# Performance work log

Hardware: AMD Instinct MI355X
Metric: run time of the kernel (lower is better)

The kernel has to match this reference:

```python
import jax, jax.numpy as jnp
import numpy as np

T, D, F_, E, K = 8192, 1024, 4096, 8, 2


def setup_inputs() -> dict:
    key = jax.random.key(0)
    ks = jax.random.split(key, 5)
    s_d = 1.0 / np.sqrt(D)
    s_f = 1.0 / np.sqrt(F_)
    return {
        "x": jax.random.normal(ks[0], (T, D), dtype=jnp.float32),
        "gate_w": jax.random.normal(ks[1], (D, E), dtype=jnp.float32) * s_d,
        "w1": jax.random.normal(ks[2], (E, D, F_), dtype=jnp.float32) * s_d,  # up (gate proj)
        "w3": jax.random.normal(ks[3], (E, D, F_), dtype=jnp.float32) * s_d,  # up (value proj)
        "w2": jax.random.normal(ks[4], (E, F_, D), dtype=jnp.float32) * s_f,  # down proj
    }


def reference(x, gate_w, w1, w2, w3):
    # gate + top-k routing
    logits = x @ gate_w                                   # [T, E]
    top_w, top_idx = jax.lax.top_k(logits, K)             # [T, K]
    w = jax.nn.softmax(top_w.astype(jnp.float32), axis=-1).astype(x.dtype)
    # combine[t, e] = routing weight of token t for expert e (0 if unrouted)
    combine = jnp.sum(w[:, :, None] * jax.nn.one_hot(top_idx, E, dtype=x.dtype), axis=1)  # [T, E]
    # dense dispatch: each expert processes all tokens, masked by combine weight
    # (identical math to the torch gather/scatter loop: unrouted tokens get weight 0)
    out = jnp.zeros_like(x)
    for e in range(E):
        h = jax.nn.silu(x @ w1[e]) * (x @ w3[e])          # [T, F] SwiGLU
        out = out + combine[:, e:e + 1] * (h @ w2[e])     # [T, D]
    return out
```

## Files before the change

kernel.cpp:

```cpp
#include <hip/hip_runtime.h>
#include <stdint.h>

#define T_TOK 8192
#define D_DIM 1024
#define F_DIM 4096
#define E_NUM 8
#define RCAP  17408
#define MT    136

typedef __bf16 bf16;
typedef __bf16 bf16x8 __attribute__((ext_vector_type(8)));
typedef float  f32x4  __attribute__((ext_vector_type(4)));

typedef const __attribute__((address_space(1))) void* gptr1;
typedef __attribute__((address_space(3))) void* lptr3;

__device__ __forceinline__ void gload_lds16(const void* g, void* l) {
    __builtin_amdgcn_global_load_lds((gptr1)g, (lptr3)l, 16, 0, 0);
}

__device__ __forceinline__ unsigned short f2b(float f) {
    uint32_t u = __float_as_uint(f);
    u = (u + 0x7FFFu + ((u >> 16) & 1u)) >> 16;
    return (unsigned short)u;
}

__global__ __launch_bounds__(256) void trans_kernel(const float* __restrict__ src,
                                                    bf16* __restrict__ dst,
                                                    int R, int C, int mode) {
    __shared__ float lt[64 * 68];
    const int e  = blockIdx.z;
    const int c0 = blockIdx.x * 64;
    const int r0 = blockIdx.y * 64;
    const float* s = src + (size_t)e * R * C;
    unsigned short* dp = (unsigned short*)dst + (size_t)e * R * C * (mode ? 2 : 1);
    const int t  = threadIdx.x;
    const int tr = t >> 4;
    const int tc = (t & 15) * 4;
    #pragma unroll
    for (int rr = 0; rr < 4; ++rr) {
        const int r = tr + rr * 16;
        const float4 v = *(const float4*)(s + (size_t)(r0 + r) * C + c0 + tc);
        *(float4*)&lt[r * 68 + tc] = v;
    }
    __syncthreads();
    const int oc  = t >> 2;
    const int seg = (t & 3) * 16;
    __attribute__((aligned(16))) unsigned short ob[16];
    #pragma unroll
    for (int i = 0; i < 16; ++i) ob[i] = f2b(lt[(seg + i) * 68 + oc]);
    const int f  = c0 + oc;
    const int fr = mode ? ((f >> 5) * 64 + ((mode == 2) ? 32 : 0) + (f & 31)) : f;
    unsigned short* orow = dp + (size_t)fr * R + (r0 + seg);
    *(uint4*)(orow)     = *(const uint4*)&ob[0];
    *(uint4*)(orow + 8) = *(const uint4*)&ob[8];
}

__global__ __launch_bounds__(256) void gate_kernel(const float* __restrict__ x,
                                                   const float* __restrict__ gw,
                                                   int* __restrict__ tki,
                                                   float* __restrict__ tkw,
                                                   int* __restrict__ counts) {
    const int t    = blockIdx.x * 4 + (threadIdx.x >> 6);
    const int lane = threadIdx.x & 63;
    const float* xr = x + (size_t)t * D_DIM;
    float acc[E_NUM];
    #pragma unroll
    for (int e = 0; e < E_NUM; ++e) acc[e] = 0.f;
    for (int j = 0; j < 16; ++j) {
        const int d = lane + 64 * j;
        const float xv = xr[d];
        const float* g = gw + (size_t)d * E_NUM;
        #pragma unroll
        for (int e = 0; e < E_NUM; ++e) acc[e] += xv * g[e];
    }
    #pragma unroll
    for (int off = 32; off >= 1; off >>= 1) {
        #pragma unroll
        for (int e = 0; e < E_NUM; ++e) acc[e] += __shfl_xor(acc[e], off);
    }
    if (lane == 0) {
        int b0 = 0; float v0 = acc[0];
        #pragma unroll
        for (int e = 1; e < E_NUM; ++e) if (acc[e] > v0) { v0 = acc[e]; b0 = e; }
        int b1 = -1; float v1 = -1e30f;
        #pragma unroll
        for (int e = 0; e < E_NUM; ++e) if (e != b0 && acc[e] > v1) { v1 = acc[e]; b1 = e; }
        const float ex = expf(v1 - v0);
        const float w0 = 1.f / (1.f + ex);
        const float w1 = ex * w0;
        tki[t * 2]     = b0;  tkw[t * 2]     = w0;
        tki[t * 2 + 1] = b1;  tkw[t * 2 + 1] = w1;
        atomicAdd(&counts[b0], 1);
        atomicAdd(&counts[b1], 1);
    }
}

__global__ void scan_kernel(const int* __restrict__ counts, int* __restrict__ aoff,
                            int* __restrict__ cursor) {
    if (threadIdx.x == 0) {
        int off = 0;
        #pragma unroll
        for (int e = 0; e < E_NUM; ++e) {
            aoff[e]   = off;
            cursor[e] = off;
            off += (counts[e] + 127) & ~127;
        }
        aoff[E_NUM] = off;
    }
}

__global__ __launch_bounds__(256) void gather_kernel(const float* __restrict__ x,
                                                     const int* __restrict__ tki,
                                                     int* __restrict__ cursor,
                                                     int* __restrict__ s2r,
                                                     bf16* __restrict__ xp) {
    const int slot = blockIdx.x * 4 + (threadIdx.x >> 6);
    const int lane = threadIdx.x & 63;
    const int t = slot >> 1;
    int row = 0;
    if (lane == 0) {
        const int e = tki[slot];
        row = atomicAdd(&cursor[e], 1);
        s2r[slot] = row;
    }
    row = __shfl(row, 0);
    const float* xr = x + (size_t)t * D_DIM + lane * 16;
    unsigned short* dst = (unsigned short*)xp + (size_t)row * D_DIM + lane * 16;
    uint32_t u[8];
    #pragma unroll
    for (int q = 0; q < 4; ++q) {
        const float4 v = *(const float4*)(xr + q * 4);
        u[q * 2]     = (uint32_t)f2b(v.x) | ((uint32_t)f2b(v.y) << 16);
        u[q * 2 + 1] = (uint32_t)f2b(v.z) | ((uint32_t)f2b(v.w) << 16);
    }
    ((uint4*)dst)[0] = make_uint4(u[0], u[1], u[2], u[3]);
    ((uint4*)dst)[1] = make_uint4(u[4], u[5], u[6], u[7]);
}

__global__ __launch_bounds__(512, 2) void gemm1_kernel(const bf16* __restrict__ xp,
                                                       const bf16* __restrict__ wb13t,
                                                       bf16* __restrict__ hb,
                                                       const int* __restrict__ aoff,
                                                       const int* __restrict__ counts) {
    __shared__ __align__(16) char As[65536];
    __shared__ __align__(16) char Bs[65536];

    const int nt = blockIdx.x;
    int bm = blockIdx.y;
    int e  = 0;
    for (; e < E_NUM; ++e) {
        const int nbi = (counts[e] + 255) >> 8;
        if (bm < nbi) break;
        bm -= nbi;
    }
    if (e >= E_NUM) return;
    const int m_base = aoff[e] + bm * 256;
    const int row_hi = aoff[e + 1];

    const int tid  = threadIdx.x;
    const int w    = tid >> 6;
    const int lane = tid & 63;
    const int wm   = w >> 2;
    const int wn   = w & 3;

    const int    lsub = lane >> 3;
    const size_t swz  = (size_t)(((lane & 7) ^ lsub) << 3);
    const bf16* Ag = xp    + (size_t)m_base * D_DIM;
    const bf16* Bg = wb13t + ((size_t)e * (2 * F_DIM) + (size_t)nt * 256) * D_DIM;
    char* sAd = As + w * 2048 + lane * 16;
    char* sBd = Bs + w * 2048 + lane * 16;
    const int rst = w * 16 + lsub;

#define G1_STAGE_A(cc, kt, h)                                                         \
    do {                                                                              \
        const size_t kcol = (size_t)(kt) * 64 + swz;                                  \
        gload_lds16(Ag + (size_t)((h) * 128 + rst) * D_DIM + kcol,                    \
                    sAd + (cc) * 32768 + (h) * 16384);                                \
        gload_lds16(Ag + (size_t)((h) * 128 + rst + 8) * D_DIM + kcol,                \
                    sAd + (cc) * 32768 + (h) * 16384 + 1024);                         \
    } while (0)
#define G1_STAGE_B(cc, kt, h)                                                         \
    do {                                                                              \
        const size_t kcol = (size_t)(kt) * 64 + swz;                                  \
        gload_lds16(Bg + (size_t)((h) * 128 + rst) * D_DIM + kcol,                    \
                    sBd + (cc) * 32768 + (h) * 16384);                                \
        gload_lds16(Bg + (size_t)((h) * 128 + rst + 8) * D_DIM + kcol,                \
                    sBd + (cc) * 32768 + (h) * 16384 + 1024);                         \
    } while (0)

    const int fm  = lane & 15;
    const int kq  = lane >> 4;
    const int kg0 = ((kq       ^ (fm & 7)) << 4);
    const int kg1 = (((4 | kq) ^ (fm & 7)) << 4);
    const char* Arb = As + wm * 16384 + fm * 128;
    const char* Brb = Bs + (wn >> 1) * 16384 + ((wn & 1) * 64 + fm) * 128;

    f32x4 acc[8][4] = {};
    bf16x8 aF[4][2], b0F[2][2], b1F[2][2];

    G1_STAGE_A(0, 0, 0); G1_STAGE_A(0, 0, 1);
    G1_STAGE_B(0, 0, 0); G1_STAGE_B(0, 0, 1);
    G1_STAGE_B(1, 1, 0); G1_STAGE_B(1, 1, 1);
    asm volatile("s_waitcnt vmcnt(4)" ::: "memory");
    __builtin_amdgcn_s_barrier();
    __builtin_amdgcn_sched_barrier(0);

    for (int u = 0; u < D_DIM / 64; ++u) {
        const int c = u & 1;
        const char* Ar = Arb + c * 32768;
        const char* Br = Brb + c * 32768;

        #pragma unroll
        for (int i = 0; i < 4; ++i) {
            aF[i][0] = *(const bf16x8*)(Ar + i * 2048 + kg0);
            aF[i][1] = *(const bf16x8*)(Ar + i * 2048 + kg1);
        }
        #pragma unroll
        for (int j = 0; j < 2; ++j) {
            b0F[j][0] = *(const bf16x8*)(Br + j * 2048 + kg0);
            b0F[j][1] = *(const bf16x8*)(Br + j * 2048 + kg1);
        }
        if (u + 1 < D_DIM / 64) G1_STAGE_A(c ^ 1, u + 1, 0);
        __builtin_amdgcn_s_barrier();
        asm volatile("s_waitcnt lgkmcnt(0)" ::: "memory");
        __builtin_amdgcn_s_setprio(1);
        #pragma unroll
        for (int i = 0; i < 4; ++i)
            #pragma unroll
            for (int j = 0; j < 2; ++j) {
                acc[i][j] = __builtin_amdgcn_mfma_f32_16x16x32_bf16(aF[i][0], b0F[j][0], acc[i][j], 0, 0, 0);
                acc[i][j] = __builtin_amdgcn_mfma_f32_16x16x32_bf16(aF[i][1], b0F[j][1], acc[i][j], 0, 0, 0);
            }
        __builtin_amdgcn_s_setprio(0);
        __builtin_amdgcn_s_barrier();

        #pragma unroll
        for (int j = 0; j < 2; ++j) {
            b1F[j][0] = *(const bf16x8*)(Br + (j + 2) * 2048 + kg0);
            b1F[j][1] = *(const bf16x8*)(Br + (j + 2) * 2048 + kg1);
        }
        if (u + 1 < D_DIM / 64) G1_STAGE_A(c ^ 1, u + 1, 1);
        __builtin_amdgcn_s_barrier();
        asm volatile("s_waitcnt lgkmcnt(0)" ::: "memory");
        __builtin_amdgcn_s_setprio(1);
        #pragma unroll
        for (int i = 0; i < 4; ++i)
            #pragma unroll
            for (int j = 0; j < 2; ++j) {
                acc[i][j + 2] = __builtin_amdgcn_mfma_f32_16x16x32_bf16(aF[i][0], b1F[j][0], acc[i][j + 2], 0, 0, 0);
                acc[i][j + 2] = __builtin_amdgcn_mfma_f32_16x16x32_bf16(aF[i][1], b1F[j][1], acc[i][j + 2], 0, 0, 0);
            }
        __builtin_amdgcn_s_setprio(0);
        __builtin_amdgcn_s_barrier();

        #pragma unroll
        for (int i = 0; i < 4; ++i) {
            aF[i][0] = *(const bf16x8*)(Ar + (i + 4) * 2048 + kg0);
            aF[i][1] = *(const bf16x8*)(Ar + (i + 4) * 2048 + kg1);
        }
        if (u + 2 < D_DIM / 64) G1_STAGE_B(c, u + 2, 0);
        __builtin_amdgcn_s_barrier();
        asm volatile("s_waitcnt lgkmcnt(0)" ::: "memory");
        __builtin_amdgcn_s_setprio(1);
        #pragma unroll
        for (int i = 0; i < 4; ++i)
            #pragma unroll
            for (int j = 0; j < 2; ++j) {
                acc[i + 4][j] = __builtin_amdgcn_mfma_f32_16x16x32_bf16(aF[i][0], b0F[j][0], acc[i + 4][j], 0, 0, 0);
                acc[i + 4][j] = __builtin_amdgcn_mfma_f32_16x16x32_bf16(aF[i][1], b0F[j][1], acc[i + 4][j], 0, 0, 0);
            }
        __builtin_amdgcn_s_setprio(0);
        __builtin_amdgcn_s_barrier();

        if (u + 2 < D_DIM / 64) G1_STAGE_B(c, u + 2, 1);
        __builtin_amdgcn_s_setprio(1);
        #pragma unroll
        for (int i = 0; i < 4; ++i)
            #pragma unroll
            for (int j = 0; j < 2; ++j) {
                acc[i + 4][j + 2] = __builtin_amdgcn_mfma_f32_16x16x32_bf16(aF[i][0], b1F[j][0], acc[i + 4][j + 2], 0, 0, 0);
                acc[i + 4][j + 2] = __builtin_amdgcn_mfma_f32_16x16x32_bf16(aF[i][1], b1F[j][1], acc[i + 4][j + 2], 0, 0, 0);
            }
        __builtin_amdgcn_s_setprio(0);

        if (u == D_DIM / 64 - 1) break;
        if (u + 2 < D_DIM / 64) {
            asm volatile("s_waitcnt vmcnt(4)" ::: "memory");
        } else {
            asm volatile("s_waitcnt vmcnt(0)" ::: "memory");
        }
        __builtin_amdgcn_s_barrier();
        __builtin_amdgcn_sched_barrier(0);
    }

    unsigned short* hw = (unsigned short*)hb;
    const int g    = nt * 4 + wn;
    const int colb = g * 32 + fm;
    const int rb0  = m_base + wm * 128 + (kq << 2);
    #pragma unroll
    for (int i = 0; i < 8; ++i) {
        #pragma unroll
        for (int r = 0; r < 4; ++r) {
            const int row = rb0 + i * 16 + r;
            if (row < row_hi) {
                #pragma unroll
                for (int jj = 0; jj < 2; ++jj) {
                    const float s1 = acc[i][jj][r];
                    const float s3 = acc[i][jj + 2][r];
                    const float hv = (s1 / (1.0f + __expf(-s1))) * s3;
                    hw[(size_t)row * F_DIM + colb + jj * 16] = f2b(hv);
                }
            }
        }
    }
#undef G1_STAGE_A
#undef G1_STAGE_B
}

__global__ __launch_bounds__(256, 2) void gemm2_kernel(const bf16* __restrict__ hb,
                                                       const bf16* __restrict__ wb2t,
                                                       float* __restrict__ yb,
                                                       const int* __restrict__ aoff,
                                                       const int* __restrict__ counts) {
    __shared__ __align__(16) bf16 As[128 * 64];
    __shared__ __align__(16) bf16 Bs[128 * 64];

    const int flat    = blockIdx.y * 8 + blockIdx.x;
    const int logical = (flat & 7) * 136 + (flat >> 3);
    const int nt      = logical & 7;
    const int m_base  = (logical >> 3) * 128;

    int e = 0;
    #pragma unroll
    for (int i = 1; i < E_NUM; ++i) if (m_base >= aoff[i]) e = i;
    if (m_base - aoff[e] >= counts[e]) return;

    const int tid  = threadIdx.x;
    const int w    = tid >> 6;
    const int lane = tid & 63;
    const int wm   = w & 1, wn = w >> 1;

    const bf16* Ab = hb + (size_t)m_base * F_DIM;
    const bf16* Bb = wb2t + ((size_t)e * D_DIM + (size_t)nt * 128) * F_DIM;

    const int lsub = lane >> 3;
    const int swzc = ((lane & 7) ^ lsub) * 8;
    const int rst  = w * 32 + lsub;
    bf16* sAd = As + w * 2048;
    bf16* sBd = Bs + w * 2048;

    const int fm  = lane & 15;
    const int kq  = lane >> 4;
    const int sl0 = ((kq    ) ^ (fm & 7)) * 8;
    const int sl1 = ((kq | 4) ^ (fm & 7)) * 8;

    f32x4 acc[4][4] = {};

    for (int kt = 0; kt < F_DIM / 64; ++kt) {
        const int k0 = kt * 64;
        #pragma unroll
        for (int j = 0; j < 4; ++j) {
            gload_lds16(Ab + (size_t)(rst + j * 8) * F_DIM + (k0 + swzc), sAd + j * 512);
            gload_lds16(Bb + (size_t)(rst + j * 8) * F_DIM + (k0 + swzc), sBd + j * 512);
        }
        __syncthreads();
        bf16x8 af[4][2], bfr[4][2];
        #pragma unroll
        for (int i = 0; i < 4; ++i) {
            const int ar = (wm * 64 + i * 16 + fm) * 64;
            const int br = (wn * 64 + i * 16 + fm) * 64;
            af[i][0]  = *(const bf16x8*)&As[ar + sl0];
            af[i][1]  = *(const bf16x8*)&As[ar + sl1];
            bfr[i][0] = *(const bf16x8*)&Bs[br + sl0];
            bfr[i][1] = *(const bf16x8*)&Bs[br + sl1];
        }
        #pragma unroll
        for (int i = 0; i < 4; ++i) {
            #pragma unroll
            for (int jn = 0; jn < 4; ++jn) {
                acc[i][jn] = __builtin_amdgcn_mfma_f32_16x16x32_bf16(af[i][0], bfr[jn][0], acc[i][jn], 0, 0, 0);
                acc[i][jn] = __builtin_amdgcn_mfma_f32_16x16x32_bf16(af[i][1], bfr[jn][1], acc[i][jn], 0, 0, 0);
            }
        }
        __syncthreads();
    }

    #pragma unroll
    for (int i = 0; i < 4; ++i) {
        const int rb = m_base + wm * 64 + i * 16 + (lane >> 4) * 4;
        #pragma unroll
        for (int r = 0; r < 4; ++r) {
            float* yrow = yb + (size_t)(rb + r) * D_DIM;
            #pragma unroll
            for (int jn = 0; jn < 4; ++jn) {
                const int col = nt * 128 + wn * 64 + jn * 16 + (lane & 15);
                yrow[col] = acc[i][jn][r];
            }
        }
    }
}

__global__ __launch_bounds__(256) void combine_kernel(const float* __restrict__ yb,
                                                      const int* __restrict__ s2r,
                                                      const float* __restrict__ tkw,
                                                      float* __restrict__ out) {
    const int idx = blockIdx.x * 256 + threadIdx.x;
    const int t = idx >> 8;
    const int c = (idx & 255) * 4;
    const int r0 = s2r[t * 2], r1 = s2r[t * 2 + 1];
    const float w0 = tkw[t * 2], w1 = tkw[t * 2 + 1];
    const float4 a = *(const float4*)(yb + (size_t)r0 * D_DIM + c);
    const float4 b = *(const float4*)(yb + (size_t)r1 * D_DIM + c);
    float4 o;
    o.x = w0 * a.x + w1 * b.x;
    o.y = w0 * a.y + w1 * b.y;
    o.z = w0 * a.z + w1 * b.z;
    o.w = w0 * a.w + w1 * b.w;
    *(float4*)(out + (size_t)t * D_DIM + c) = o;
}

extern "C" void kernel_launch(void* const* d_in, const int* in_sizes, int n_in,
                              void* d_out, int out_size, void* d_ws, size_t ws_size,
                              hipStream_t stream) {
    const float* x  = (const float*)d_in[0];
    const float* gw = (const float*)d_in[1];
    const float* w1 = (const float*)d_in[2];
    const float* w3 = (const float*)d_in[3];
    const float* w2 = (const float*)d_in[4];
    float* out = (float*)d_out;

    char* ws = (char*)d_ws;
    bf16*  wb13t = (bf16*)(ws);
    bf16*  wb2t  = (bf16*)(ws);
    float* yb    = (float*)(ws + (size_t)67108864);
    bf16*  xp    = (bf16*)(ws + (size_t)134217728);
    size_t off   = (size_t)134217728 + (size_t)RCAP * D_DIM * 2;
    bf16*  hb    = (bf16*)(ws + off); off += (size_t)RCAP * F_DIM * 2;
    int*   tki = (int*)(ws + off);   off += (size_t)T_TOK * 2 * 4;
    float* tkw = (float*)(ws + off); off += (size_t)T_TOK * 2 * 4;
    int* counts = (int*)(ws + off);  off += 64;
    int* cursor = (int*)(ws + off);  off += 64;
    int* aoff   = (int*)(ws + off);  off += 64;
    int* s2r    = (int*)(ws + off);  off += (size_t)T_TOK * 2 * 4;

    hipMemsetAsync(counts, 0, 64, stream);

    gate_kernel<<<T_TOK / 4, 256, 0, stream>>>(x, gw, tki, tkw, counts);
    scan_kernel<<<1, 64, 0, stream>>>(counts, aoff, cursor);
    gather_kernel<<<(T_TOK * 2) / 4, 256, 0, stream>>>(x, tki, cursor, s2r, xp);

    trans_kernel<<<dim3(F_DIM / 64, D_DIM / 64, E_NUM), 256, 0, stream>>>(w1, wb13t, D_DIM, F_DIM, 1);
    trans_kernel<<<dim3(F_DIM / 64, D_DIM / 64, E_NUM), 256, 0, stream>>>(w3, wb13t, D_DIM, F_DIM, 2);

    gemm1_kernel<<<dim3(2 * F_DIM / 256, 72), 512, 0, stream>>>(xp, wb13t, hb, aoff, counts);

    trans_kernel<<<dim3(D_DIM / 64, F_DIM / 64, E_NUM), 256, 0, stream>>>(w2, wb2t, F_DIM, D_DIM, 0);

    gemm2_kernel<<<dim3(D_DIM / 128, MT), 256, 0, stream>>>(hb, wb2t, yb, aoff, counts);

    combine_kernel<<<(T_TOK * 256) / 256, 256, 0, stream>>>(yb, s2r, tkw, out);
}
```

Baseline: 1.345 ms.

## Rewrite down-projection GEMM with 256x256 tiles and double-buffered pipelined loads

The second grouped GEMM moves from a 128x128 tile with 256 threads and a single LDS buffer to a 256x256 tile with 512 threads, like the first GEMM. Two LDS stages are filled by async global-to-LDS loads that are issued between MFMA phases. Barriers and priority hints interleave the loads with compute, and rows are masked by the end of each expert's range. This is meant to raise operand reuse and hide memory latency. In exchange it uses much more LDS per block, and expert segments are padded to 256 rows, so some blocks do wasted work.

```diff
diff --git a/kernel.cpp b/kernel.cpp
--- a/kernel.cpp
+++ b/kernel.cpp
@@ -318,87 +318,181 @@
 #undef G1_STAGE_B
 }
 
-__global__ __launch_bounds__(256, 2) void gemm2_kernel(const bf16* __restrict__ hb,
+__global__ __launch_bounds__(512, 2) void gemm2_kernel(const bf16* __restrict__ hb,
                                                        const bf16* __restrict__ wb2t,
                                                        float* __restrict__ yb,
                                                        const int* __restrict__ aoff,
                                                        const int* __restrict__ counts) {
-    __shared__ __align__(16) bf16 As[128 * 64];
-    __shared__ __align__(16) bf16 Bs[128 * 64];
-
-    const int flat    = blockIdx.y * 8 + blockIdx.x;
-    const int logical = (flat & 7) * 136 + (flat >> 3);
-    const int nt      = logical & 7;
-    const int m_base  = (logical >> 3) * 128;
-
-    int e = 0;
-    #pragma unroll
-    for (int i = 1; i < E_NUM; ++i) if (m_base >= aoff[i]) e = i;
-    if (m_base - aoff[e] >= counts[e]) return;
+    __shared__ __align__(16) char As[65536];
+    __shared__ __align__(16) char Bs[65536];
+
+    const int nt = blockIdx.x;
+    int bm = blockIdx.y;
+    int e  = 0;
+    for (; e < E_NUM; ++e) {
+        const int nbi = (counts[e] + 255) >> 8;
+        if (bm < nbi) break;
+        bm -= nbi;
+    }
+    if (e >= E_NUM) return;
+    const int m_base = aoff[e] + bm * 256;
+    const int row_hi = aoff[e + 1];
 
     const int tid  = threadIdx.x;
     const int w    = tid >> 6;
     const int lane = tid & 63;
-    const int wm   = w & 1, wn = w >> 1;
-
-    const bf16* Ab = hb + (size_t)m_base * F_DIM;
-    const bf16* Bb = wb2t + ((size_t)e * D_DIM + (size_t)nt * 128) * F_DIM;
-
-    const int lsub = lane >> 3;
-    const int swzc = ((lane & 7) ^ lsub) * 8;
-    const int rst  = w * 32 + lsub;
-    bf16* sAd = As + w * 2048;
-    bf16* sBd = Bs + w * 2048;
+    const int wm   = w >> 2;
+    const int wn   = w & 3;
+
+    const int    lsub = lane >> 3;
+    const size_t swz  = (size_t)(((lane & 7) ^ lsub) << 3);
+    const bf16* Ag = hb   + (size_t)m_base * F_DIM;
+    const bf16* Bg = wb2t + ((size_t)e * D_DIM + (size_t)nt * 256) * F_DIM;
+    char* sAd = As + w * 2048 + lane * 16;
+    char* sBd = Bs + w * 2048 + lane * 16;
+    const int rst = w * 16 + lsub;
+
+#define G2_STAGE_A(cc, kt, h)                                                         \
+    do {                                                                              \
+        const size_t kcol = (size_t)(kt) * 64 + swz;                                  \
+        gload_lds16(Ag + (size_t)((h) * 128 + rst) * F_DIM + kcol,                    \
+                    sAd + (cc) * 32768 + (h) * 16384);                                \
+        gload_lds16(Ag + (size_t)((h) * 128 + rst + 8) * F_DIM + kcol,                \
+                    sAd + (cc) * 32768 + (h) * 16384 + 1024);                         \
+    } while (0)
+#define G2_STAGE_B(cc, kt, h)                                                         \
+    do {                                                                              \
+        const size_t kcol = (size_t)(kt) * 64 + swz;                                  \
+        gload_lds16(Bg + (size_t)((h) * 128 + rst) * F_DIM + kcol,                    \
+                    sBd + (cc) * 32768 + (h) * 16384);                                \
+        gload_lds16(Bg + (size_t)((h) * 128 + rst + 8) * F_DIM + kcol,                \
+                    sBd + (cc) * 32768 + (h) * 16384 + 1024);                         \
+    } while (0)
 
     const int fm  = lane & 15;
     const int kq  = lane >> 4;
-    const int sl0 = ((kq    ) ^ (fm & 7)) * 8;
-    const int sl1 = ((kq | 4) ^ (fm & 7)) * 8;
-
-    f32x4 acc[4][4] = {};
-
-    for (int kt = 0; kt < F_DIM / 64; ++kt) {
-        const int k0 = kt * 64;
-        #pragma unroll
-        for (int j = 0; j < 4; ++j) {
-            gload_lds16(Ab + (size_t)(rst + j * 8) * F_DIM + (k0 + swzc), sAd + j * 512);
-            gload_lds16(Bb + (size_t)(rst + j * 8) * F_DIM + (k0 + swzc), sBd + j * 512);
-        }
-        __syncthreads();
-        bf16x8 af[4][2], bfr[4][2];
+    const int kg0 = ((kq       ^ (fm & 7)) << 4);
+    const int kg1 = (((4 | kq) ^ (fm & 7)) << 4);
+    const char* Arb = As + wm * 16384 + fm * 128;
+    const char* Brb = Bs + (wn >> 1) * 16384 + ((wn & 1) * 64 + fm) * 128;
+
+    f32x4 acc[8][4] = {};
+    bf16x8 aF[4][2], b0F[2][2], b1F[2][2];
+
+    G2_STAGE_A(0, 0, 0); G2_STAGE_A(0, 0, 1);
+    G2_STAGE_B(0, 0, 0); G2_STAGE_B(0, 0, 1);
+    G2_STAGE_B(1, 1, 0); G2_STAGE_B(1, 1, 1);
+    asm volatile("s_waitcnt vmcnt(4)" ::: "memory");
+    __builtin_amdgcn_s_barrier();
+    __builtin_amdgcn_sched_barrier(0);
+
+    const int NT = F_DIM / 64;
+    for (int u = 0; u < NT; ++u) {
+        const int c = u & 1;
+        const char* Ar = Arb + c * 32768;
+        const char* Br = Brb + c * 32768;
+
         #pragma unroll
         for (int i = 0; i < 4; ++i) {
-            const int ar = (wm * 64 + i * 16 + fm) * 64;
-            const int br = (wn * 64 + i * 16 + fm) * 64;
-            af[i][0]  = *(const bf16x8*)&As[ar + sl0];
-            af[i][1]  = *(const bf16x8*)&As[ar + sl1];
-            bfr[i][0] = *(const bf16x8*)&Bs[br + sl0];
-            bfr[i][1] = *(const bf16x8*)&Bs[br + sl1];
-        }
+            aF[i][0] = *(const bf16x8*)(Ar + i * 2048 + kg0);
+            aF[i][1] = *(const bf16x8*)(Ar + i * 2048 + kg1);
+        }
+        #pragma unroll
+        for (int j = 0; j < 2; ++j) {
+            b0F[j][0] = *(const bf16x8*)(Br + j * 2048 + kg0);
+            b0F[j][1] = *(const bf16x8*)(Br + j * 2048 + kg1);
+        }
+        if (u + 1 < NT) G2_STAGE_A(c ^ 1, u + 1, 0);
+        __builtin_amdgcn_s_barrier();
+        asm volatile("s_waitcnt lgkmcnt(0)" ::: "memory");
+        __builtin_amdgcn_s_setprio(1);
+        #pragma unroll
+        for (int i = 0; i < 4; ++i)
+            #pragma unroll
+            for (int j = 0; j < 2; ++j) {
+                acc[i][j] = __builtin_amdgcn_mfma_f32_16x16x32_bf16(aF[i][0], b0F[j][0], acc[i][j], 0, 0, 0);
+                acc[i][j] = __builtin_amdgcn_mfma_f32_16x16x32_bf16(aF[i][1], b0F[j][1], acc[i][j], 0, 0, 0);
+            }
+        __builtin_amdgcn_s_setprio(0);
+        __builtin_amdgcn_s_barrier();
+
+        #pragma unroll
+        for (int j = 0; j < 2; ++j) {
+            b1F[j][0] = *(const bf16x8*)(Br + (j + 2) * 2048 + kg0);
+            b1F[j][1] = *(const bf16x8*)(Br + (j + 2) * 2048 + kg1);
+        }
+        if (u + 1 < NT) G2_STAGE_A(c ^ 1, u + 1, 1);
+        __builtin_amdgcn_s_barrier();
+        asm volatile("s_waitcnt lgkmcnt(0)" ::: "memory");
+        __builtin_amdgcn_s_setprio(1);
+        #pragma unroll
+        for (int i = 0; i < 4; ++i)
+            #pragma unroll
+            for (int j = 0; j < 2; ++j) {
+                acc[i][j + 2] = __builtin_amdgcn_mfma_f32_16x16x32_bf16(aF[i][0], b1F[j][0], acc[i][j + 2], 0, 0, 0);
+                acc[i][j + 2] = __builtin_amdgcn_mfma_f32_16x16x32_bf16(aF[i][1], b1F[j][1], acc[i][j + 2], 0, 0, 0);
+            }
+        __builtin_amdgcn_s_setprio(0);
+        __builtin_amdgcn_s_barrier();
+
         #pragma unroll
         for (int i = 0; i < 4; ++i) {
-            #pragma unroll
-            for (int jn = 0; jn < 4; ++jn) {
-                acc[i][jn] = __builtin_amdgcn_mfma_f32_16x16x32_bf16(af[i][0], bfr[jn][0], acc[i][jn], 0, 0, 0);
-                acc[i][jn] = __builtin_amdgcn_mfma_f32_16x16x32_bf16(af[i][1], bfr[jn][1], acc[i][jn], 0, 0, 0);
-            }
-        }
-        __syncthreads();
-    }
-
-    #pragma unroll
-    for (int i = 0; i < 4; ++i) {
-        const int rb = m_base + wm * 64 + i * 16 + (lane >> 4) * 4;
+            aF[i][0] = *(const bf16x8*)(Ar + (i + 4) * 2048 + kg0);
+            aF[i][1] = *(const bf16x8*)(Ar + (i + 4) * 2048 + kg1);
+        }
+        if (u + 2 < NT) G2_STAGE_B(c, u + 2, 0);
+        __builtin_amdgcn_s_barrier();
+        asm volatile("s_waitcnt lgkmcnt(0)" ::: "memory");
+        __builtin_amdgcn_s_setprio(1);
+        #pragma unroll
+        for (int i = 0; i < 4; ++i)
+            #pragma unroll
+            for (int j = 0; j < 2; ++j) {
+                acc[i + 4][j] = __builtin_amdgcn_mfma_f32_16x16x32_bf16(aF[i][0], b0F[j][0], acc[i + 4][j], 0, 0, 0);
+                acc[i + 4][j] = __builtin_amdgcn_mfma_f32_16x16x32_bf16(aF[i][1], b0F[j][1], acc[i + 4][j], 0, 0, 0);
+            }
+        __builtin_amdgcn_s_setprio(0);
+        __builtin_amdgcn_s_barrier();
+
+        if (u + 2 < NT) G2_STAGE_B(c, u + 2, 1);
+        __builtin_amdgcn_s_setprio(1);
+        #pragma unroll
+        for (int i = 0; i < 4; ++i)
+            #pragma unroll
+            for (int j = 0; j < 2; ++j) {
+                acc[i + 4][j + 2] = __builtin_amdgcn_mfma_f32_16x16x32_bf16(aF[i][0], b1F[j][0], acc[i + 4][j + 2], 0, 0, 0);
+                acc[i + 4][j + 2] = __builtin_amdgcn_mfma_f32_16x16x32_bf16(aF[i][1], b1F[j][1], acc[i + 4][j + 2], 0, 0, 0);
+            }
+        __builtin_amdgcn_s_setprio(0);
+
+        if (u == NT - 1) break;
+        if (u + 2 < NT) {
+            asm volatile("s_waitcnt vmcnt(4)" ::: "memory");
+        } else {
+            asm volatile("s_waitcnt vmcnt(0)" ::: "memory");
+        }
+        __builtin_amdgcn_s_barrier();
+        __builtin_amdgcn_sched_barrier(0);
+    }
+
+    const int colb = nt * 256 + wn * 64 + fm;
+    const int rb0  = m_base + wm * 128 + (kq << 2);
+    #pragma unroll
+    for (int i = 0; i < 8; ++i) {
         #pragma unroll
         for (int r = 0; r < 4; ++r) {
-            float* yrow = yb + (size_t)(rb + r) * D_DIM;
-            #pragma unroll
-            for (int jn = 0; jn < 4; ++jn) {
-                const int col = nt * 128 + wn * 64 + jn * 16 + (lane & 15);
-                yrow[col] = acc[i][jn][r];
-            }
-        }
-    }
+            const int row = rb0 + i * 16 + r;
+            if (row < row_hi) {
+                float* yrow = yb + (size_t)row * D_DIM;
+                #pragma unroll
+                for (int jn = 0; jn < 4; ++jn) {
+                    yrow[colb + jn * 16] = acc[i][jn][r];
+                }
+            }
+        }
+    }
+#undef G2_STAGE_A
+#undef G2_STAGE_B
 }
 
 __global__ __launch_bounds__(256) void combine_kernel(const float* __restrict__ yb,
@@ -457,7 +551,7 @@
 
     trans_kernel<<<dim3(D_DIM / 64, F_DIM / 64, E_NUM), 256, 0, stream>>>(w2, wb2t, F_DIM, D_DIM, 0);
 
-    gemm2_kernel<<<dim3(D_DIM / 128, MT), 256, 0, stream>>>(hb, wb2t, yb, aoff, counts);
+    gemm2_kernel<<<dim3(D_DIM / 256, 72), 512, 0, stream>>>(hb, wb2t, yb, aoff, counts);
 
     combine_kernel<<<(T_TOK * 256) / 256, 256, 0, stream>>>(yb, s2r, tkw, out);
 }
```

Measured after the change: 1.410 ms. +4.8%, slower.
